# Kernel tuning notes

Hardware: AMD Instinct MI355X
Metric: run time of the kernel (lower is better)

Reference implementation:

```python
import math
import jax, jax.numpy as jnp
import numpy as np

B, C, T = 4, 1024, 2048
HEADS, NDECAY = 8, 4
HD = C // HEADS  # head dim = 128


def conv1x1(x, W, b):
    # x: [B, Cin, T], W: [Cout, Cin], b: [Cout] -> [B, Cout, T]
    return jnp.einsum('oc,bct->bot', W, x) + b[None, :, None]


def setup_inputs() -> dict:
    key = jax.random.key(0)
    ks = jax.random.split(key, 7)
    s = 1.0 / math.sqrt(C)
    x = jax.random.normal(ks[0], (B, C, T), dtype=jnp.float32)
    W_content = jax.random.normal(ks[1], (C, C), dtype=jnp.float32) * s
    b_content = jnp.zeros((C,), dtype=jnp.float32)
    W_query = jax.random.normal(ks[2], (C, C), dtype=jnp.float32) * s
    b_query = jnp.zeros((C,), dtype=jnp.float32)
    W_key = jax.random.normal(ks[3], (C, C), dtype=jnp.float32) * s
    b_key = jnp.zeros((C,), dtype=jnp.float32)
    # query_decay: weight *= 0.01, bias = -2 (per __init__)
    W_qdecay = jax.random.normal(ks[4], (HEADS * NDECAY, C), dtype=jnp.float32) * s * 0.01
    b_qdecay = jnp.full((HEADS * NDECAY,), -2.0, dtype=jnp.float32)
    W_proj = jax.random.normal(ks[5], (C, C), dtype=jnp.float32) * s
    b_proj = jnp.zeros((C,), dtype=jnp.float32)
    return {
        'x': x,
        'W_content': W_content, 'b_content': b_content,
        'W_query': W_query, 'b_query': b_query,
        'W_key': W_key, 'b_key': b_key,
        'W_qdecay': W_qdecay, 'b_qdecay': b_qdecay,
        'W_proj': W_proj, 'b_proj': b_proj,
    }


def reference(x, W_content, b_content, W_query, b_query, W_key, b_key,
              W_qdecay, b_qdecay, W_proj, b_proj):
    Bx, Cx, Tx = x.shape
    queries = conv1x1(x, W_query, b_query).reshape(Bx, HEADS, HD, Tx)
    keys = conv1x1(x, W_key, b_key).reshape(Bx, HEADS, HD, Tx)
    dots = jnp.einsum('bhct,bhcs->bhts', keys, queries) / math.sqrt(HD)

    # learned decay bias: sigmoid-gated distance kernel
    idx = jnp.arange(Tx, dtype=x.dtype)
    delta = jnp.abs(idx[:, None] - idx[None, :])  # [T, T]
    decays = jnp.arange(1, NDECAY + 1, dtype=x.dtype)
    decay_q = conv1x1(x, W_qdecay, b_qdecay).reshape(Bx, HEADS, NDECAY, Tx)
    decay_q = jax.nn.sigmoid(decay_q) / 2
    decay_kernel = -decays[:, None, None] * delta[None] / math.sqrt(NDECAY)  # [f,T,T]
    dots = dots + jnp.einsum('fts,bhfs->bhts', decay_kernel, decay_q)

    eye = jnp.eye(Tx, dtype=bool)
    dots = jnp.where(eye[None, None], jnp.asarray(-100.0, dots.dtype), dots)
    weights = jax.nn.softmax(dots, axis=2)  # softmax over t (dim=2), matching torch

    content = conv1x1(x, W_content, b_content).reshape(Bx, HEADS, HD, Tx)
    result = jnp.einsum('bhts,bhct->bhcs', weights, content).reshape(Bx, -1, Tx)
    return x + conv1x1(result, W_proj, b_proj)
```

## Files before the change

### kernel.cpp

```cpp
#include <hip/hip_runtime.h>
#include <hip/hip_bf16.h>
#include <type_traits>


typedef short bf16x8 __attribute__((ext_vector_type(8)));
typedef float f32x4 __attribute__((ext_vector_type(4)));
typedef float f32x16 __attribute__((ext_vector_type(16)));

#define DI __device__ __forceinline__

constexpr int Bc = 4, Cc = 1024, Tc = 2048, Hc = 8, HDc = 128;

DI void gload16(const void* g, void* lds) {
  __builtin_amdgcn_global_load_lds((const __attribute__((address_space(1))) unsigned int*)g,
                                   (__attribute__((address_space(3))) unsigned int*)lds,
                                   16, 0, 0);
}

DI unsigned cvtpk_bf16(float lo, float hi) {
  unsigned d;
  asm("v_cvt_pk_bf16_f32 %0, %1, %2" : "=v"(d) : "v"(lo), "v"(hi));
  return d;
}

DI float max3f(float a, float b, float c) {
  float d;
  asm("v_max3_f32 %0, %1, %2, %3" : "=v"(d) : "v"(a), "v"(b), "v"(c));
  return d;
}

DI f32x16 mfma32(bf16x8 a, bf16x8 b, f32x16 c) {
  return __builtin_amdgcn_mfma_f32_32x32x16_bf16(a, b, c, 0, 0, 0);
}

__global__ __launch_bounds__(256) void k_cast_w(
    const float* __restrict__ wc, const float* __restrict__ wq, const float* __restrict__ wk,
    const float* __restrict__ wp, const float* __restrict__ wqd,
    __hip_bfloat16* __restrict__ owc, __hip_bfloat16* __restrict__ owq,
    __hip_bfloat16* __restrict__ owk, __hip_bfloat16* __restrict__ owp,
    __hip_bfloat16* __restrict__ owqd) {
  int g = blockIdx.x * 256 + threadIdx.x;
  const float* src; __hip_bfloat16* dst; int base;
  if (g < 262144)       { src = wc;  dst = owc;  base = 0; }
  else if (g < 524288)  { src = wq;  dst = owq;  base = 262144; }
  else if (g < 786432)  { src = wk;  dst = owk;  base = 524288; }
  else if (g < 1048576) { src = wp;  dst = owp;  base = 786432; }
  else                  { src = wqd; dst = owqd; base = 1048576; }
  int idx = (g - base) * 4;
  float4 v = *(const float4*)(src + idx);
  union { __hip_bfloat16 h[4]; uint2 u; } pk;
  pk.h[0] = __float2bfloat16(v.x); pk.h[1] = __float2bfloat16(v.y);
  pk.h[2] = __float2bfloat16(v.z); pk.h[3] = __float2bfloat16(v.w);
  *(uint2*)(dst + idx) = pk.u;
}

__global__ __launch_bounds__(256) void k_xt(const float* __restrict__ x,
                                            __hip_bfloat16* __restrict__ xt) {
  const int b = blockIdx.z, c0 = blockIdx.y * 64;
  const int w = threadIdx.x >> 6, lane = threadIdx.x & 63;
  const int t = blockIdx.x * 256 + w * 64 + lane;
  const float* xb = x + (size_t)b * Cc * Tc;
  __hip_bfloat16* xo = xt + ((size_t)b * Tc + t) * Cc;
  #pragma unroll
  for (int c = c0; c < c0 + 64; c += 8) {
    union { __hip_bfloat16 h[8]; uint4 u4; } pk;
    #pragma unroll
    for (int uu = 0; uu < 8; ++uu)
      pk.h[uu] = __float2bfloat16(xb[(size_t)(c + uu) * Tc + t]);
    *(uint4*)(xo + c) = pk.u4;
  }
}

__global__ __launch_bounds__(128) void k_decay(
    const __hip_bfloat16* __restrict__ wqd, const float* __restrict__ bqd,
    const __hip_bfloat16* __restrict__ xt, float* __restrict__ G) {
  const int b = blockIdx.y;
  const int w = threadIdx.x >> 6, lane = threadIdx.x & 63, lo = lane & 15, hi = lane >> 4;
  const int t0 = blockIdx.x * 32 + w * 16;
  const __hip_bfloat16* xb = xt + ((size_t)b * Tc + t0 + lo) * Cc;
  f32x4 acc[2] = {};
  for (int k0 = 0; k0 < Cc; k0 += 32) {
    bf16x8 bb = *(const bf16x8*)(xb + k0 + hi * 8);
    #pragma unroll
    for (int mi = 0; mi < 2; ++mi) {
      bf16x8 a = *(const bf16x8*)(wqd + (size_t)(mi * 16 + lo) * Cc + k0 + hi * 8);
      acc[mi] = __builtin_amdgcn_mfma_f32_16x16x32_bf16(a, bb, acc[mi], 0, 0, 0);
    }
  }
  #pragma unroll
  for (int mi = 0; mi < 2; ++mi) {
    const int h = mi * 4 + hi;
    float g = 0.f;
    #pragma unroll
    for (int r = 0; r < 4; ++r) {
      const float dq = acc[mi][r] + bqd[mi * 16 + hi * 4 + r];
      const float sg = 1.f / (1.f + __expf(-dq));
      g += (float)(r + 1) * sg * 0.25f;
    }
    G[((size_t)b * Hc + h) * Tc + t0 + lo] = g * 1.4426950408889634f;
  }
}

__global__ __launch_bounds__(256, 2) void k_gemm_qkv(
    const __hip_bfloat16* __restrict__ wc, const __hip_bfloat16* __restrict__ wq,
    const __hip_bfloat16* __restrict__ wk,
    const float* __restrict__ bc, const float* __restrict__ bq, const float* __restrict__ bk,
    const __hip_bfloat16* __restrict__ xt,
    __hip_bfloat16* __restrict__ V, __hip_bfloat16* __restrict__ Qtr,
    __hip_bfloat16* __restrict__ Ktr) {
  __shared__ char smem[32768];
  const int b = blockIdx.z, mt = blockIdx.y, n0 = blockIdx.x * 128;
  const int mode = mt >> 3, m0 = (mt & 7) * 128;
  const __hip_bfloat16* A = (mode == 0) ? wc : (mode == 1 ? wq : wk);
  const float* bias = (mode == 0) ? bc : (mode == 1 ? bq : bk);
  const __hip_bfloat16* Bt = xt + (size_t)b * Tc * Cc;
  const int tid = threadIdx.x, lane = tid & 63, lo = lane & 15, hi = lane >> 4;
  const int w = tid >> 6, wm = w >> 1, wn = w & 1;
  f32x4 acc[4][4] = {};

  auto stage = [&](int buf, int k0) {
    #pragma unroll
    for (int q = 0; q < 2; ++q) {
      int ci = tid + q * 256;
      gload16(A + (size_t)(m0 + (ci >> 2)) * Cc + k0 + (ci & 3) * 8,
              smem + buf * 8192 + ci * 16);
    }
    #pragma unroll
    for (int q = 0; q < 2; ++q) {
      int ci = tid + q * 256;
      gload16(Bt + (size_t)(n0 + (ci >> 2)) * Cc + k0 + (ci & 3) * 8,
              smem + 16384 + buf * 8192 + ci * 16);
    }
  };

  stage(0, 0);
  __syncthreads();
  for (int kt = 0; kt < 32; ++kt) {
    const int buf = kt & 1;
    if (kt + 1 < 32) stage(buf ^ 1, (kt + 1) * 32);
    const char* Ab = smem + buf * 8192;
    const char* Bb = smem + 16384 + buf * 8192;
    bf16x8 af[4], bfr[4];
    #pragma unroll
    for (int mi = 0; mi < 4; ++mi)
      af[mi] = *(const bf16x8*)(Ab + (wm * 64 + mi * 16 + lo) * 64 + hi * 16);
    #pragma unroll
    for (int ni = 0; ni < 4; ++ni)
      bfr[ni] = *(const bf16x8*)(Bb + (wn * 64 + ni * 16 + lo) * 64 + hi * 16);
    #pragma unroll
    for (int mi = 0; mi < 4; ++mi)
      #pragma unroll
      for (int ni = 0; ni < 4; ++ni)
        acc[mi][ni] = __builtin_amdgcn_mfma_f32_16x16x32_bf16(af[mi], bfr[ni], acc[mi][ni], 0, 0, 0);
    __syncthreads();
  }

  if (mode == 0) {
    #pragma unroll
    for (int mi = 0; mi < 4; ++mi) {
      const int ob = m0 + wm * 64 + mi * 16 + hi * 4;
      float b4[4];
      #pragma unroll
      for (int r = 0; r < 4; ++r) b4[r] = bias[ob + r];
      #pragma unroll
      for (int ni = 0; ni < 4; ++ni) {
        const int t = n0 + wn * 64 + ni * 16 + lo;
        #pragma unroll
        for (int r = 0; r < 4; ++r)
          V[((size_t)b * Cc + ob + r) * Tc + t] = __float2bfloat16(acc[mi][ni][r] + b4[r]);
      }
    }
  } else {
    __hip_bfloat16* dst = (mode == 1) ? Qtr : Ktr;
    const float sc = (mode == 1) ? 0.12751744416f : 1.0f;
    #pragma unroll
    for (int mi = 0; mi < 4; ++mi) {
      const int ob = m0 + wm * 64 + mi * 16 + hi * 4;
      const int h = ob >> 7, c = ob & 127;
      float b4[4];
      #pragma unroll
      for (int r = 0; r < 4; ++r) b4[r] = bias[ob + r];
      #pragma unroll
      for (int ni = 0; ni < 4; ++ni) {
        const int t = n0 + wn * 64 + ni * 16 + lo;
        union { __hip_bfloat16 hh[4]; uint2 u; } pk;
        #pragma unroll
        for (int r = 0; r < 4; ++r)
          pk.hh[r] = __float2bfloat16((acc[mi][ni][r] + b4[r]) * sc);
        *(uint2*)(dst + (((size_t)b * Hc + h) * Tc + t) * HDc + c) = pk.u;
      }
    }
  }
}

__global__ __launch_bounds__(256, 2) void k_attn(
    const __hip_bfloat16* __restrict__ Qtr, const __hip_bfloat16* __restrict__ Ktr,
    const __hip_bfloat16* __restrict__ Vv, const float* __restrict__ G,
    __hip_bfloat16* __restrict__ Ot) {
  __shared__ char smem[65536];
  const int wg = blockIdx.x;
  const int bh = (wg & 7) + 8 * ((wg >> 3) & 3);
  const int sb = wg >> 5;
  const int b = bh >> 3, h = bh & 7;
  const int tid = threadIdx.x, w = tid >> 6, lane = tid & 63;
  const int l31 = lane & 31, pl = lane >> 5;
  const int sw = sb * 128 + w * 32;
  const int sq = sw + l31;
  const __hip_bfloat16* Qb = Qtr + (size_t)bh * Tc * HDc;
  const __hip_bfloat16* Kb = Ktr + (size_t)bh * Tc * HDc;
  const __hip_bfloat16* Vb = Vv + (size_t)bh * HDc * Tc;

  const float g = G[(size_t)bh * Tc + sq];

  bf16x8 qf[8];
  #pragma unroll
  for (int kk = 0; kk < 8; ++kk)
    qf[kk] = *(const bf16x8*)(Qb + (size_t)sq * HDc + kk * 16 + pl * 8);

  int kbo[8], vbo[4];
  const int swz = (l31 & 7) * 16;
  #pragma unroll
  for (int kk = 0; kk < 8; ++kk) {
    const int c = kk * 2 + pl;
    kbo[kk] = l31 * 256 + (c & 8) * 16 + (((c & 7) * 16) ^ swz);
  }
  #pragma unroll
  for (int ks = 0; ks < 4; ++ks)
    vbo[ks] = 16384 + l31 * 128 + (((ks * 2 + pl) * 16) ^ swz);

  const __hip_bfloat16* kgp[4];
  const __hip_bfloat16* vgp[4];
  #pragma unroll
  for (int q = 0; q < 4; ++q) {
    const int ci = tid + q * 256;
    const int tt_ = ci >> 4, d = (ci & 15) ^ (tt_ & 7);
    kgp[q] = Kb + (size_t)tt_ * HDc + d * 8;
    const int cc = ci >> 3, d2 = (ci & 7) ^ (cc & 7);
    vgp[q] = Vb + (size_t)cc * Tc + d2 * 8;
  }

  const short onebf = 0x3f80;
  const bf16x8 onesv = {onebf, onebf, onebf, onebf, onebf, onebf, onebf, onebf};

  float m_ = -100000.f;
  f32x16 oacc[4] = {};
  f32x16 lacc = {};

  auto stage = [&](auto bufc) {
    constexpr int BUF = decltype(bufc)::value;
    #pragma unroll
    for (int q = 0; q < 4; ++q)
      gload16(kgp[q], smem + BUF * 32768 + (tid + q * 256) * 16);
    #pragma unroll
    for (int q = 0; q < 4; ++q)
      gload16(vgp[q], smem + BUF * 32768 + 16384 + (tid + q * 256) * 16);
    #pragma unroll
    for (int q = 0; q < 4; ++q) { kgp[q] += 64 * HDc; vgp[q] += 64; }
  };

  auto tile_compute = [&](auto bufc, int T0) {
    constexpr int BUF = decltype(bufc)::value;
    f32x16 stv0 = {}, stv1 = {};
    #pragma unroll
    for (int kk = 0; kk < 8; ++kk) {
      bf16x8 kf0 = *(const bf16x8*)(smem + BUF * 32768 + kbo[kk]);
      bf16x8 kf1 = *(const bf16x8*)(smem + BUF * 32768 + 8192 + kbo[kk]);
      stv0 = mfma32(kf0, qf[kk], stv0);
      stv1 = mfma32(kf1, qf[kk], stv1);
    }

    if (T0 >= sw + 32 || T0 + 64 <= sw) {
      const float a = (T0 >= sw + 32) ? -g : g;
      const float base0 = __builtin_fmaf(a, (float)(T0 + 4 * pl - sq), -m_);
      const float base1 = __builtin_fmaf(a, 32.f, base0);
      #pragma unroll
      for (int r = 0; r < 16; ++r) {
        const float c = (float)((r & 3) + 8 * (r >> 2));
        stv0[r] += __builtin_fmaf(a, c, base0);
        stv1[r] += __builtin_fmaf(a, c, base1);
      }
    } else {
      const float isq = (float)(T0 + 4 * pl - sq);
      #pragma unroll
      for (int r = 0; r < 16; ++r) {
        const float c = (float)((r & 3) + 8 * (r >> 2));
        const float d0 = isq + c;
        stv0[r] = __builtin_fmaf(-fabsf(d0), g, stv0[r] - m_);
        stv1[r] = __builtin_fmaf(-fabsf(d0 + 32.f), g, stv1[r] - m_);
      }
      #pragma unroll
      for (int r = 0; r < 16; ++r) {
        const int tr = T0 + (r & 3) + 8 * (r >> 2) + 4 * pl;
        if (tr == sq) stv0[r] = -100000.f;
        if (tr + 32 == sq) stv1[r] = -100000.f;
      }
    }

    float tm = fmaxf(stv0[0], stv1[0]);
    #pragma unroll
    for (int r = 1; r < 16; ++r) tm = max3f(tm, stv0[r], stv1[r]);
    tm = fmaxf(tm, __shfl_xor(tm, 32, 64));
    if (!__all(tm <= 8.f)) {
      const float d = fmaxf(tm, 0.f);
      m_ += d;
      const float al = exp2f(-d);
      #pragma unroll
      for (int cb = 0; cb < 4; ++cb)
        #pragma unroll
        for (int r = 0; r < 16; ++r) oacc[cb][r] *= al;
      lacc[0] *= al;
      #pragma unroll
      for (int r = 0; r < 16; ++r) { stv0[r] -= d; stv1[r] -= d; }
    }
    #pragma unroll
    for (int r = 0; r < 16; ++r) {
      stv0[r] = exp2f(stv0[r]);
      stv1[r] = exp2f(stv1[r]);
    }

    bf16x8 pf[4];
    #pragma unroll
    for (int ks = 0; ks < 4; ++ks) {
      const f32x16& sv = (ks < 2) ? stv0 : stv1;
      const int qe = (2 * ks) & 3, qo = qe + 1;
      unsigned E0 = cvtpk_bf16(sv[4 * qe + 0], sv[4 * qe + 1]);
      unsigned E1 = cvtpk_bf16(sv[4 * qe + 2], sv[4 * qe + 3]);
      unsigned O0 = cvtpk_bf16(sv[4 * qo + 0], sv[4 * qo + 1]);
      unsigned O1 = cvtpk_bf16(sv[4 * qo + 2], sv[4 * qo + 3]);
      asm("v_permlane32_swap_b32 %0, %1" : "+v"(E0), "+v"(O0));
      asm("v_permlane32_swap_b32 %0, %1" : "+v"(E1), "+v"(O1));
      union { unsigned u[4]; bf16x8 v; } pk;
      pk.u[0] = E0; pk.u[1] = E1; pk.u[2] = O0; pk.u[3] = O1;
      pf[ks] = pk.v;
    }

    #pragma unroll
    for (int ks = 0; ks < 4; ++ks) {
      #pragma unroll
      for (int cb = 0; cb < 4; ++cb) {
        bf16x8 vf = *(const bf16x8*)(smem + BUF * 32768 + cb * 4096 + vbo[ks]);
        oacc[cb] = mfma32(vf, pf[ks], oacc[cb]);
      }
      lacc = mfma32(onesv, pf[ks], lacc);
    }
  };

  std::integral_constant<int, 0> ic0;
  std::integral_constant<int, 1> ic1;

  stage(ic0);
  __syncthreads();
  #pragma unroll 1
  for (int tt = 0; tt < 16; ++tt) {
    stage(ic1);
    tile_compute(ic0, tt * 128);
    __syncthreads();
    if (tt < 15) stage(ic0);
    tile_compute(ic1, tt * 128 + 64);
    __syncthreads();
  }

  const float linv = 1.f / lacc[0];
  __hip_bfloat16* Orow = Ot + ((size_t)b * Tc + sq) * Cc + h * HDc;
  #pragma unroll
  for (int cb = 0; cb < 4; ++cb)
    #pragma unroll
    for (int q = 0; q < 4; ++q) {
      union { __hip_bfloat16 hh[4]; uint2 u; } pk;
      #pragma unroll
      for (int rr = 0; rr < 4; ++rr)
        pk.hh[rr] = __float2bfloat16(oacc[cb][4 * q + rr] * linv);
      *(uint2*)(Orow + cb * 32 + 8 * q + 4 * pl) = pk.u;
    }
}

__global__ __launch_bounds__(256, 2) void k_proj(
    const __hip_bfloat16* __restrict__ wp, const float* __restrict__ bp,
    const __hip_bfloat16* __restrict__ Ot, const float* __restrict__ x,
    float* __restrict__ out) {
  __shared__ char smem[32768];
  const int b = blockIdx.z, m0 = blockIdx.y * 128, n0 = blockIdx.x * 128;
  const __hip_bfloat16* Bt = Ot + (size_t)b * Tc * Cc;
  const int tid = threadIdx.x, lane = tid & 63, lo = lane & 15, hi = lane >> 4;
  const int w = tid >> 6, wm = w >> 1, wn = w & 1;
  f32x4 acc[4][4] = {};

  auto stage = [&](int buf, int k0) {
    #pragma unroll
    for (int q = 0; q < 2; ++q) {
      int ci = tid + q * 256;
      gload16(wp + (size_t)(m0 + (ci >> 2)) * Cc + k0 + (ci & 3) * 8,
              smem + buf * 8192 + ci * 16);
    }
    #pragma unroll
    for (int q = 0; q < 2; ++q) {
      int ci = tid + q * 256;
      gload16(Bt + (size_t)(n0 + (ci >> 2)) * Cc + k0 + (ci & 3) * 8,
              smem + 16384 + buf * 8192 + ci * 16);
    }
  };

  stage(0, 0);
  __syncthreads();
  for (int kt = 0; kt < 32; ++kt) {
    const int buf = kt & 1;
    if (kt + 1 < 32) stage(buf ^ 1, (kt + 1) * 32);
    const char* Ab = smem + buf * 8192;
    const char* Bb = smem + 16384 + buf * 8192;
    bf16x8 af[4], bfr[4];
    #pragma unroll
    for (int mi = 0; mi < 4; ++mi)
      af[mi] = *(const bf16x8*)(Ab + (wm * 64 + mi * 16 + lo) * 64 + hi * 16);
    #pragma unroll
    for (int ni = 0; ni < 4; ++ni)
      bfr[ni] = *(const bf16x8*)(Bb + (wn * 64 + ni * 16 + lo) * 64 + hi * 16);
    #pragma unroll
    for (int mi = 0; mi < 4; ++mi)
      #pragma unroll
      for (int ni = 0; ni < 4; ++ni)
        acc[mi][ni] = __builtin_amdgcn_mfma_f32_16x16x32_bf16(af[mi], bfr[ni], acc[mi][ni], 0, 0, 0);
    __syncthreads();
  }

  #pragma unroll
  for (int mi = 0; mi < 4; ++mi) {
    const int ob = m0 + wm * 64 + mi * 16 + hi * 4;
    float b4[4];
    #pragma unroll
    for (int r = 0; r < 4; ++r) b4[r] = bp[ob + r];
    #pragma unroll
    for (int ni = 0; ni < 4; ++ni) {
      const int t = n0 + wn * 64 + ni * 16 + lo;
      #pragma unroll
      for (int r = 0; r < 4; ++r) {
        const size_t o = ((size_t)b * Cc + ob + r) * Tc + t;
        out[o] = acc[mi][ni][r] + b4[r] + x[o];
      }
    }
  }
}

extern "C" void kernel_launch(void* const* d_in, const int* in_sizes, int n_in,
                              void* d_out, int out_size, void* d_ws, size_t ws_size,
                              hipStream_t stream) {
  const float* x   = (const float*)d_in[0];
  const float* Wc  = (const float*)d_in[1];
  const float* bc  = (const float*)d_in[2];
  const float* Wq  = (const float*)d_in[3];
  const float* bq  = (const float*)d_in[4];
  const float* Wk  = (const float*)d_in[5];
  const float* bk  = (const float*)d_in[6];
  const float* Wqd = (const float*)d_in[7];
  const float* bqd = (const float*)d_in[8];
  const float* Wp  = (const float*)d_in[9];
  const float* bp  = (const float*)d_in[10];
  float* out = (float*)d_out;

  char* ws = (char*)d_ws;
  size_t off = 0;
  auto alloc = [&](size_t n) { char* p = ws + off; off += (n + 255) & ~(size_t)255; return p; };
  __hip_bfloat16* xt   = (__hip_bfloat16*)alloc((size_t)Bc * Tc * Cc * 2);
  __hip_bfloat16* wcb  = (__hip_bfloat16*)alloc((size_t)1024 * 1024 * 2);
  __hip_bfloat16* wqb  = (__hip_bfloat16*)alloc((size_t)1024 * 1024 * 2);
  __hip_bfloat16* wkb  = (__hip_bfloat16*)alloc((size_t)1024 * 1024 * 2);
  __hip_bfloat16* wpb  = (__hip_bfloat16*)alloc((size_t)1024 * 1024 * 2);
  __hip_bfloat16* wqdb = (__hip_bfloat16*)alloc((size_t)32 * 1024 * 2);
  __hip_bfloat16* Qtr  = (__hip_bfloat16*)alloc((size_t)Bc * Hc * Tc * HDc * 2);
  __hip_bfloat16* Ktr  = (__hip_bfloat16*)alloc((size_t)Bc * Hc * Tc * HDc * 2);
  __hip_bfloat16* Vv   = (__hip_bfloat16*)alloc((size_t)Bc * Hc * HDc * Tc * 2);
  float* G             = (float*)alloc((size_t)Bc * Hc * Tc * 4);
  __hip_bfloat16* Ot = xt;

  k_cast_w<<<dim3(4128), 256, 0, stream>>>(Wc, Wq, Wk, Wp, Wqd, wcb, wqb, wkb, wpb, wqdb);
  k_xt<<<dim3(Tc / 256, Cc / 64, Bc), 256, 0, stream>>>(x, xt);
  k_decay<<<dim3(Tc / 32, Bc), 128, 0, stream>>>(wqdb, bqd, xt, G);
  k_gemm_qkv<<<dim3(Tc / 128, 24, Bc), 256, 0, stream>>>(wcb, wqb, wkb, bc, bq, bk, xt,
                                                         Vv, Qtr, Ktr);
  k_attn<<<dim3(512), 256, 0, stream>>>(Qtr, Ktr, Vv, G, Ot);
  k_proj<<<dim3(Tc / 128, Cc / 128, Bc), 256, 0, stream>>>(wpb, bp, Ot, x, out);
}
```

Baseline: 316.3 us.

## Merge prep kernels, reorder attention tiles near-diagonal first, raise GEMM occupancy

Merges the weight-cast and x-transpose kernels into one launch, which saves one kernel launch. The attention loop now visits key tiles starting at the query block's diagonal and walking outward, so the running max settles early and rescaling happens less often. Stage addressing becomes index-based instead of incrementing pointers. exp2f is swapped for the hardware exp2 builtin. Launch bounds for the QKV and projection GEMMs rise from 2 to 3 waves per SIMD, which may force register spills.

```diff
diff --git a/kernel.cpp b/kernel.cpp
--- a/kernel.cpp
+++ b/kernel.cpp
@@ -29,45 +29,50 @@
   return d;
 }
 
+DI float fexp2(float x) { return __builtin_amdgcn_exp2f(x); }
+
 DI f32x16 mfma32(bf16x8 a, bf16x8 b, f32x16 c) {
   return __builtin_amdgcn_mfma_f32_32x32x16_bf16(a, b, c, 0, 0, 0);
 }
 
-__global__ __launch_bounds__(256) void k_cast_w(
+__global__ __launch_bounds__(256) void k_prep(
+    const float* __restrict__ x,
     const float* __restrict__ wc, const float* __restrict__ wq, const float* __restrict__ wk,
     const float* __restrict__ wp, const float* __restrict__ wqd,
+    __hip_bfloat16* __restrict__ xt,
     __hip_bfloat16* __restrict__ owc, __hip_bfloat16* __restrict__ owq,
     __hip_bfloat16* __restrict__ owk, __hip_bfloat16* __restrict__ owp,
     __hip_bfloat16* __restrict__ owqd) {
-  int g = blockIdx.x * 256 + threadIdx.x;
-  const float* src; __hip_bfloat16* dst; int base;
-  if (g < 262144)       { src = wc;  dst = owc;  base = 0; }
-  else if (g < 524288)  { src = wq;  dst = owq;  base = 262144; }
-  else if (g < 786432)  { src = wk;  dst = owk;  base = 524288; }
-  else if (g < 1048576) { src = wp;  dst = owp;  base = 786432; }
-  else                  { src = wqd; dst = owqd; base = 1048576; }
-  int idx = (g - base) * 4;
-  float4 v = *(const float4*)(src + idx);
-  union { __hip_bfloat16 h[4]; uint2 u; } pk;
-  pk.h[0] = __float2bfloat16(v.x); pk.h[1] = __float2bfloat16(v.y);
-  pk.h[2] = __float2bfloat16(v.z); pk.h[3] = __float2bfloat16(v.w);
-  *(uint2*)(dst + idx) = pk.u;
-}
-
-__global__ __launch_bounds__(256) void k_xt(const float* __restrict__ x,
-                                            __hip_bfloat16* __restrict__ xt) {
-  const int b = blockIdx.z, c0 = blockIdx.y * 64;
-  const int w = threadIdx.x >> 6, lane = threadIdx.x & 63;
-  const int t = blockIdx.x * 256 + w * 64 + lane;
-  const float* xb = x + (size_t)b * Cc * Tc;
-  __hip_bfloat16* xo = xt + ((size_t)b * Tc + t) * Cc;
-  #pragma unroll
-  for (int c = c0; c < c0 + 64; c += 8) {
-    union { __hip_bfloat16 h[8]; uint4 u4; } pk;
-    #pragma unroll
-    for (int uu = 0; uu < 8; ++uu)
-      pk.h[uu] = __float2bfloat16(xb[(size_t)(c + uu) * Tc + t]);
-    *(uint4*)(xo + c) = pk.u4;
+  const int bid = blockIdx.x;
+  if (bid < 4128) {
+    int g = bid * 256 + threadIdx.x;
+    const float* src; __hip_bfloat16* dst; int base;
+    if (g < 262144)       { src = wc;  dst = owc;  base = 0; }
+    else if (g < 524288)  { src = wq;  dst = owq;  base = 262144; }
+    else if (g < 786432)  { src = wk;  dst = owk;  base = 524288; }
+    else if (g < 1048576) { src = wp;  dst = owp;  base = 786432; }
+    else                  { src = wqd; dst = owqd; base = 1048576; }
+    int idx = (g - base) * 4;
+    float4 v = *(const float4*)(src + idx);
+    union { __hip_bfloat16 h[4]; uint2 u; } pk;
+    pk.h[0] = __float2bfloat16(v.x); pk.h[1] = __float2bfloat16(v.y);
+    pk.h[2] = __float2bfloat16(v.z); pk.h[3] = __float2bfloat16(v.w);
+    *(uint2*)(dst + idx) = pk.u;
+  } else {
+    const int bid2 = bid - 4128;
+    const int b = bid2 >> 7, c0 = ((bid2 >> 3) & 15) * 64;
+    const int w = threadIdx.x >> 6, lane = threadIdx.x & 63;
+    const int t = (bid2 & 7) * 256 + w * 64 + lane;
+    const float* xb = x + (size_t)b * Cc * Tc;
+    __hip_bfloat16* xo = xt + ((size_t)b * Tc + t) * Cc;
+    #pragma unroll
+    for (int c = c0; c < c0 + 64; c += 8) {
+      union { __hip_bfloat16 h[8]; uint4 u4; } pk;
+      #pragma unroll
+      for (int uu = 0; uu < 8; ++uu)
+        pk.h[uu] = __float2bfloat16(xb[(size_t)(c + uu) * Tc + t]);
+      *(uint4*)(xo + c) = pk.u4;
+    }
   }
 }
 
@@ -101,7 +106,7 @@
   }
 }
 
-__global__ __launch_bounds__(256, 2) void k_gemm_qkv(
+__global__ __launch_bounds__(256, 3) void k_gemm_qkv(
     const __hip_bfloat16* __restrict__ wc, const __hip_bfloat16* __restrict__ wq,
     const __hip_bfloat16* __restrict__ wk,
     const float* __restrict__ bc, const float* __restrict__ bq, const float* __restrict__ bk,
@@ -206,6 +211,7 @@
   const int l31 = lane & 31, pl = lane >> 5;
   const int sw = sb * 128 + w * 32;
   const int sq = sw + l31;
+  const int d1 = 2 * sb + 1;
   const __hip_bfloat16* Qb = Qtr + (size_t)bh * Tc * HDc;
   const __hip_bfloat16* Kb = Ktr + (size_t)bh * Tc * HDc;
   const __hip_bfloat16* Vb = Vv + (size_t)bh * HDc * Tc;
@@ -246,16 +252,16 @@
   f32x16 oacc[4] = {};
   f32x16 lacc = {};
 
-  auto stage = [&](auto bufc) {
+  auto stage = [&](auto bufc, int ti) {
     constexpr int BUF = decltype(bufc)::value;
+    const size_t ko = (size_t)ti * 64 * HDc;
+    const int vo = ti * 64;
     #pragma unroll
     for (int q = 0; q < 4; ++q)
-      gload16(kgp[q], smem + BUF * 32768 + (tid + q * 256) * 16);
+      gload16(kgp[q] + ko, smem + BUF * 32768 + (tid + q * 256) * 16);
     #pragma unroll
     for (int q = 0; q < 4; ++q)
-      gload16(vgp[q], smem + BUF * 32768 + 16384 + (tid + q * 256) * 16);
-    #pragma unroll
-    for (int q = 0; q < 4; ++q) { kgp[q] += 64 * HDc; vgp[q] += 64; }
+      gload16(vgp[q] + vo, smem + BUF * 32768 + 16384 + (tid + q * 256) * 16);
   };
 
   auto tile_compute = [&](auto bufc, int T0) {
@@ -303,7 +309,7 @@
     if (!__all(tm <= 8.f)) {
       const float d = fmaxf(tm, 0.f);
       m_ += d;
-      const float al = exp2f(-d);
+      const float al = fexp2(-d);
       #pragma unroll
       for (int cb = 0; cb < 4; ++cb)
         #pragma unroll
@@ -314,8 +320,8 @@
     }
     #pragma unroll
     for (int r = 0; r < 16; ++r) {
-      stv0[r] = exp2f(stv0[r]);
-      stv1[r] = exp2f(stv1[r]);
+      stv0[r] = fexp2(stv0[r]);
+      stv1[r] = fexp2(stv1[r]);
     }
 
     bf16x8 pf[4];
@@ -347,16 +353,17 @@
 
   std::integral_constant<int, 0> ic0;
   std::integral_constant<int, 1> ic1;
-
-  stage(ic0);
+  auto t0i = [&](int j) { return (j <= d1) ? (d1 - j) : j; };
+
+  stage(ic0, t0i(0));
   __syncthreads();
   #pragma unroll 1
-  for (int tt = 0; tt < 16; ++tt) {
-    stage(ic1);
-    tile_compute(ic0, tt * 128);
+  for (int i = 0; i < 32; i += 2) {
+    stage(ic1, t0i(i + 1));
+    tile_compute(ic0, t0i(i) * 64);
     __syncthreads();
-    if (tt < 15) stage(ic0);
-    tile_compute(ic1, tt * 128 + 64);
+    if (i + 2 < 32) stage(ic0, t0i(i + 2));
+    tile_compute(ic1, t0i(i + 1) * 64);
     __syncthreads();
   }
 
@@ -374,7 +381,7 @@
     }
 }
 
-__global__ __launch_bounds__(256, 2) void k_proj(
+__global__ __launch_bounds__(256, 3) void k_proj(
     const __hip_bfloat16* __restrict__ wp, const float* __restrict__ bp,
     const __hip_bfloat16* __restrict__ Ot, const float* __restrict__ x,
     float* __restrict__ out) {
@@ -471,8 +478,8 @@
   float* G             = (float*)alloc((size_t)Bc * Hc * Tc * 4);
   __hip_bfloat16* Ot = xt;
 
-  k_cast_w<<<dim3(4128), 256, 0, stream>>>(Wc, Wq, Wk, Wp, Wqd, wcb, wqb, wkb, wpb, wqdb);
-  k_xt<<<dim3(Tc / 256, Cc / 64, Bc), 256, 0, stream>>>(x, xt);
+  k_prep<<<dim3(4640), 256, 0, stream>>>(x, Wc, Wq, Wk, Wp, Wqd, xt,
+                                         wcb, wqb, wkb, wpb, wqdb);
   k_decay<<<dim3(Tc / 32, Bc), 128, 0, stream>>>(wqdb, bqd, xt, G);
   k_gemm_qkv<<<dim3(Tc / 128, 24, Bc), 256, 0, stream>>>(wcb, wqb, wkb, bc, bq, bk, xt,
                                                          Vv, Qtr, Ktr);
```

Result: faster. 301.2 us (-4.8%).
